# Optimization experiments

Hardware: AMD Instinct MI355X
Metric: run time of the kernel (lower is better)

Reference implementation:

```python
import jax, jax.numpy as jnp
import numpy as np

N = 100000      # nodes
E = 1600000     # edges (avg degree 16)
IN = 128
OUT = 256


def setup_inputs() -> dict:
    key = jax.random.key(0)
    ks = jax.random.split(key, 8)
    x = jax.random.normal(ks[0], (N, IN), dtype=jnp.float32)
    edge_index = jax.random.randint(ks[1], (2, E), 0, N, dtype=jnp.int64)
    # GCNConv weights (glorot-ish scale) and biases
    W1 = jax.random.normal(ks[2], (IN, OUT), dtype=jnp.float32) / np.float32(np.sqrt(IN))
    b1 = jnp.zeros((OUT,), jnp.float32)
    W2 = jax.random.normal(ks[3], (OUT, OUT), dtype=jnp.float32) / np.float32(np.sqrt(OUT))
    b2 = jnp.zeros((OUT,), jnp.float32)
    # projection Linear(IN, OUT)
    Wp = jax.random.normal(ks[4], (IN, OUT), dtype=jnp.float32) / np.float32(np.sqrt(IN))
    bp = jax.random.normal(ks[5], (OUT,), dtype=jnp.float32) * 0.01
    return {"x": x, "edge_index": edge_index, "W1": W1, "b1": b1,
            "W2": W2, "b2": b2, "Wp": Wp, "bp": bp}


def _gcn_conv(x, W, b, src, dst, n):
    """PyG GCNConv: D^{-1/2}(A+I)D^{-1/2} X W + b. src/dst already include self-loops."""
    xw = x @ W                                              # [n, out]
    ones = jnp.ones(src.shape[0], dtype=xw.dtype)
    deg = jax.ops.segment_sum(ones, dst, num_segments=n)    # in-degree incl. self-loop
    dinv = jnp.where(deg > 0, jax.lax.rsqrt(deg), 0.0)
    norm = dinv[src] * dinv[dst]                            # [e]
    msgs = xw[src] * norm[:, None]                          # gather + scale
    out = jax.ops.segment_sum(msgs, dst, num_segments=n)    # scatter-add
    return out + b


def reference(x, edge_index, W1, b1, W2, b2, Wp, bp):
    n = x.shape[0]
    loop = jnp.arange(n, dtype=edge_index.dtype)            # self-loops
    src = jnp.concatenate([edge_index[0], loop])
    dst = jnp.concatenate([edge_index[1], loop])
    out = jax.nn.relu(_gcn_conv(x, W1, b1, src, dst, n))
    out = _gcn_conv(out, W2, b2, src, dst, n)
    identity = x @ Wp + bp                                  # projection (IN != OUT)
    return jax.nn.relu(out + identity)
```

## Files before the change

kernel.cpp:

```cpp
#include <hip/hip_runtime.h>

#define NODES 100000
#define EDGES 1600000
#define FIN   128
#define FOUT  256
#define NBUCK 196
#define NBLKS 98

typedef __bf16 bf16;
typedef __bf16 bf16x8 __attribute__((ext_vector_type(8)));
typedef __bf16 bf16x4 __attribute__((ext_vector_type(4)));
typedef __bf16 bf16x2 __attribute__((ext_vector_type(2)));
typedef float  f32x4  __attribute__((ext_vector_type(4)));
typedef float  f32x2  __attribute__((ext_vector_type(2)));

__device__ __forceinline__ f32x2 bf2f(unsigned w) {
    f32x2 r;
    r[0] = __uint_as_float(w << 16);
    r[1] = __uint_as_float(w & 0xffff0000u);
    return r;
}

__device__ __forceinline__ void acc_u4(f32x2 a[4], uint4 w) {
    a[0] += bf2f(w.x); a[1] += bf2f(w.y);
    a[2] += bf2f(w.z); a[3] += bf2f(w.w);
}

__device__ __forceinline__ int edge_at(const int* __restrict__ ei, int which, int i,
                                       int is64) {
    if (is64) return ei[2 * (which * EDGES + i)];
    return ei[which * EDGES + i];
}

__global__ __launch_bounds__(256) void init_kernel(const void* __restrict__ x,
                                                   const int* __restrict__ ei,
                                                   int* __restrict__ zero0,
                                                   int* __restrict__ flags,
                                                   float* __restrict__ zpadA,
                                                   float* __restrict__ zpadB) {
    int b = blockIdx.x, t = threadIdx.x;
    if (b < 394) {
        int i = b * 256 + t;
        if (i < 100864) zero0[i] = 0;
        return;
    }
    zpadA[t] = 0.0f;
    zpadB[t] = 0.0f;
    __shared__ int s_f32_evidence;
    __shared__ int s_odd_nonzero;
    if (t == 0) { s_f32_evidence = 0; s_odd_nonzero = 0; }
    __syncthreads();
    const bf16* xb = (const bf16*)x;
    int local_f32 = 0;
    for (int i = t; i < 4096; i += 256) {
        float v = fabsf((float)xb[i]);
        if (!(v < 1e4f)) local_f32 = 1;
    }
    if (local_f32) atomicOr(&s_f32_evidence, 1);
    int local_odd = 0;
    for (int k = t; k < 1024; k += 256) {
        if (ei[2 * k + 1] != 0) local_odd = 1;
    }
    if (local_odd) atomicOr(&s_odd_nonzero, 1);
    __syncthreads();
    if (t == 0) {
        flags[0] = s_f32_evidence ? 0 : 1;
        flags[1] = s_odd_nonzero ? 0 : 1;
    }
}

__global__ __launch_bounds__(512) void degcnt_pack(const int* __restrict__ ei,
                                                   int* __restrict__ deg,
                                                   int* __restrict__ bhist,
                                                   const void* __restrict__ W1,
                                                   const void* __restrict__ W2,
                                                   const void* __restrict__ Wp,
                                                   const void* __restrict__ b1,
                                                   const void* __restrict__ b2,
                                                   const void* __restrict__ bp,
                                                   bf16* __restrict__ W1p, bf16* __restrict__ W2p,
                                                   bf16* __restrict__ Wpp, bf16* __restrict__ b1b,
                                                   bf16* __restrict__ b2b, bf16* __restrict__ bpb,
                                                   const int* __restrict__ flags) {
    if (blockIdx.x < 3125) {
        __shared__ int lh[256];
        int t = threadIdx.x;
        if (t < 256) lh[t] = 0;
        __syncthreads();
        int i = blockIdx.x * 512 + t;
        if (i < EDGES) {
            int is64 = flags[1];
            int s = edge_at(ei, 0, i, is64);
            int d = edge_at(ei, 1, i, is64);
            if (s >= 0 && s < NODES && d >= 0 && d < NODES) {
                atomicAdd(&deg[d], 1);
                atomicAdd(&lh[d >> 9], 1);
            }
        }
        __syncthreads();
        if (t < NBUCK && lh[t] > 0) atomicAdd(&bhist[t], lh[t]);
        return;
    }
    if (threadIdx.x >= 256) return;
    int fl = flags[0];
    int b = blockIdx.x - 3125;
    if (b < 512) {
        const void* W; bf16* Wo; int idx;
        if (b < 128)      { W = W1; Wo = W1p; idx = b * 256 + threadIdx.x; }
        else if (b < 384) { W = W2; Wo = W2p; idx = (b - 128) * 256 + threadIdx.x; }
        else              { W = Wp; Wo = Wpp; idx = (b - 384) * 256 + threadIdx.x; }
        int j    = idx & 7;
        int lane = (idx >> 3) & 63;
        int ct   = (idx >> 9) & 15;
        int kt   = idx >> 13;
        int k = kt * 32 + (lane >> 4) * 8 + j;
        int n = ct * 16 + (lane & 15);
        Wo[idx] = fl ? ((const bf16*)W)[k * 256 + n]
                     : (bf16)(((const float*)W)[k * 256 + n]);
    } else {
        const void* bb; bf16* bo;
        if (b == 512)      { bb = b1; bo = b1b; }
        else if (b == 513) { bb = b2; bo = b2b; }
        else               { bb = bp; bo = bpb; }
        int i = threadIdx.x;
        bo[i] = fl ? ((const bf16*)bb)[i] : (bf16)(((const float*)bb)[i]);
    }
}

__global__ __launch_bounds__(1024) void scan1(const int* __restrict__ deg,
                                              int* __restrict__ col_ptr,
                                              int* __restrict__ blksum, int n) {
    __shared__ int sm[1024];
    int t = threadIdx.x;
    int i = blockIdx.x * 1024 + t;
    int v = (i < n) ? deg[i] + 1 : 0;
    sm[t] = v;
    __syncthreads();
    for (int off = 1; off < 1024; off <<= 1) {
        int u = (t >= off) ? sm[t - off] : 0;
        __syncthreads();
        sm[t] += u;
        __syncthreads();
    }
    if (i <= n) col_ptr[i] = sm[t] - v;
    if (t == 1023) blksum[blockIdx.x] = sm[t];
}

#define EPB 4096
__global__ __launch_bounds__(256) void part_scan3(const int* __restrict__ ei,
                                                  const int* __restrict__ bhist,
                                                  int* __restrict__ bcur,
                                                  uint2* __restrict__ pairs,
                                                  const int* __restrict__ flags,
                                                  int* __restrict__ col_ptr,
                                                  const int* __restrict__ blk,
                                                  const int* __restrict__ deg,
                                                  float* __restrict__ dinv,
                                                  int* __restrict__ col_idx, int n) {
    if (blockIdx.x < 391) {
        __shared__ int lh[256], sc[256], lst[256], lcu[256], gb[256], bs[256];
        __shared__ uint2 stage[EPB];
        int t = threadIdx.x;
        int base = blockIdx.x * EPB;
        int is64 = flags[1];

        lh[t] = 0;
        __syncthreads();

        int es[16], ed[16];
#pragma unroll
        for (int j = 0; j < 16; ++j) {
            int i = base + j * 256 + t;
            int s = -1, d = -1;
            if (i < EDGES) {
                s = edge_at(ei, 0, i, is64);
                d = edge_at(ei, 1, i, is64);
                if (s < 0 || s >= NODES || d < 0 || d >= NODES) d = -1;
            }
            es[j] = s; ed[j] = d;
            if (d >= 0) atomicAdd(&lh[d >> 9], 1);
        }
        __syncthreads();
        sc[t] = lh[t];
        __syncthreads();
        for (int off = 1; off < 256; off <<= 1) {
            int u = (t >= off) ? sc[t - off] : 0;
            __syncthreads();
            sc[t] += u;
            __syncthreads();
        }
        int start = sc[t] - lh[t];
        lst[t] = start;
        lcu[t] = start;
        __syncthreads();
#pragma unroll
        for (int j = 0; j < 16; ++j) {
            if (ed[j] >= 0) {
                int p = atomicAdd(&lcu[ed[j] >> 9], 1);
                stage[p] = make_uint2((unsigned)es[j], (unsigned)ed[j]);
            }
        }
        __syncthreads();
        int v2 = (t < NBUCK) ? bhist[t] : 0;
        bs[t] = v2;
        __syncthreads();
        for (int off = 1; off < 256; off <<= 1) {
            int u = (t >= off) ? bs[t - off] : 0;
            __syncthreads();
            bs[t] += u;
            __syncthreads();
        }
        if (t < NBUCK && lh[t] > 0)
            gb[t] = (bs[t] - v2) + atomicAdd(&bcur[t], lh[t]);
        __syncthreads();
        int nval = sc[255];
        for (int slot = t; slot < nval; slot += 256) {
            uint2 e = stage[slot];
            int b = (int)(e.y >> 9);
            pairs[(size_t)gb[b] + (slot - lst[b])] = e;
        }
        return;
    }
    __shared__ int sb[128];
    int t = threadIdx.x;
    int sid = blockIdx.x - 391;
    int ov = 0;
    if (t < 128) { ov = (t < NBLKS) ? blk[t] : 0; sb[t] = ov; }
    __syncthreads();
    for (int off = 1; off < 128; off <<= 1) {
        int u = (t >= off && t < 128) ? sb[t - off] : 0;
        __syncthreads();
        if (t < 128) sb[t] += u;
        __syncthreads();
    }
    if (t < 128) sb[t] -= ov;
    __syncthreads();
    int i = sid * 256 + t;
    if (i <= n) {
        int v = col_ptr[i] + sb[i >> 10];
        col_ptr[i] = v;
        if (i < n) col_idx[v] = i;
    }
    if (i < n) dinv[i] = rsqrtf((float)deg[i] + 1.0f);
}

__global__ __launch_bounds__(256) void ff_proj(const uint2* __restrict__ pairs,
                                               const int* __restrict__ bhist,
                                               const int* __restrict__ col_ptr,
                                               int* __restrict__ col_idx,
                                               const void* __restrict__ Av,
                                               const bf16* __restrict__ Wpk,
                                               const float* __restrict__ dinv,
                                               const bf16* __restrict__ biasp,
                                               const bf16* __restrict__ bias2,
                                               void* __restrict__ outv,
                                               bf16* __restrict__ projb,
                                               int use_projb,
                                               bf16* __restrict__ Xs,
                                               const int* __restrict__ flags) {
    if (blockIdx.x < NBUCK) {
        __shared__ int lcur[512];
        __shared__ int bs2[256];
        int b = blockIdx.x;
        int t = threadIdx.x;
        int v2 = (t < NBUCK) ? bhist[t] : 0;
        bs2[t] = v2;
        __syncthreads();
        for (int off = 1; off < 256; off <<= 1) {
            int u = (t >= off) ? bs2[t - off] : 0;
            __syncthreads();
            bs2[t] += u;
            __syncthreads();
        }
        int be = bs2[b];
        int bb = be - bhist[b];
        int node = (b << 9) + t;
        lcur[t] = (node < NODES) ? col_ptr[node] + 1 : 0;
        int node2 = node + 256;
        lcur[t + 256] = (node2 < NODES) ? col_ptr[node2] + 1 : 0;
        __syncthreads();
        for (int i = bb + t; i < be; i += 256) {
            uint2 e = pairs[i];
            int pos = atomicAdd(&lcur[e.y & 511], 1);
            col_idx[pos] = (int)e.x;
        }
        return;
    }
    int a_f32 = (flags[0] == 0);
    int wave = threadIdx.x >> 6;
    int lane = threadIdx.x & 63;
    int row0 = (blockIdx.x - NBUCK) * 64;
    int lr = lane & 15;
    int lk = (lane >> 4) * 8;

    int arow[4];
    float di4[4];
#pragma unroll
    for (int rf = 0; rf < 4; ++rf) {
        int r = row0 + rf * 16 + lr;
        arow[rf] = r < NODES ? r : (NODES - 1);
        di4[rf] = dinv[arow[rf]];
    }

    f32x4 acc[4][4];
    f32x4 z = {0.f, 0.f, 0.f, 0.f};
#pragma unroll
    for (int i = 0; i < 4; ++i)
#pragma unroll
        for (int j = 0; j < 4; ++j) acc[i][j] = z;

    for (int kt = 0; kt < 4; ++kt) {
        bf16x8 af[4];
        if (!a_f32) {
            const bf16* Ab = (const bf16*)Av + kt * 32 + lk;
#pragma unroll
            for (int rf = 0; rf < 4; ++rf)
                af[rf] = *(const bf16x8*)(Ab + (size_t)arow[rf] * FIN);
        } else {
            const float* Af = (const float*)Av + kt * 32 + lk;
#pragma unroll
            for (int rf = 0; rf < 4; ++rf) {
                const float* p = Af + (size_t)arow[rf] * FIN;
                f32x4 lo = *(const f32x4*)p;
                f32x4 hi = *(const f32x4*)(p + 4);
                af[rf][0] = (bf16)lo[0]; af[rf][1] = (bf16)lo[1];
                af[rf][2] = (bf16)lo[2]; af[rf][3] = (bf16)lo[3];
                af[rf][4] = (bf16)hi[0]; af[rf][5] = (bf16)hi[1];
                af[rf][6] = (bf16)hi[2]; af[rf][7] = (bf16)hi[3];
            }
        }
#pragma unroll
        for (int rf = 0; rf < 4; ++rf) {
            bf16x8 xsv;
#pragma unroll
            for (int j = 0; j < 8; ++j) xsv[j] = (bf16)(di4[rf] * (float)af[rf][j]);
            *(bf16x8*)(Xs + (size_t)arow[rf] * FIN + kt * 32 + lk) = xsv;
        }
        const bf16* wb = Wpk + ((size_t)(kt * 16 + wave * 4) * 64 + lane) * 8;
        bf16x8 bfv[4];
#pragma unroll
        for (int cf = 0; cf < 4; ++cf)
            bfv[cf] = *(const bf16x8*)(wb + cf * 512);
#pragma unroll
        for (int rf = 0; rf < 4; ++rf)
#pragma unroll
            for (int cf = 0; cf < 4; ++cf)
                acc[rf][cf] = __builtin_amdgcn_mfma_f32_16x16x32_bf16(
                    af[rf], bfv[cf], acc[rf][cf], 0, 0, 0);
    }

    int rb = (lane >> 4) * 4;
#pragma unroll
    for (int rf = 0; rf < 4; ++rf) {
#pragma unroll
        for (int r = 0; r < 4; ++r) {
            int row = row0 + rf * 16 + rb + r;
            if (row >= NODES) continue;
#pragma unroll
            for (int cf = 0; cf < 4; ++cf) {
                int col = wave * 64 + cf * 16 + lr;
                float v = acc[rf][cf][r] + (float)biasp[col] + (float)bias2[col];
                size_t off = (size_t)row * 256 + col;
                if (a_f32) {
                    if (use_projb) projb[off] = (bf16)v;
                    else           ((float*)outv)[off] = v;
                } else {
                    ((bf16*)outv)[off] = (bf16)v;
                }
            }
        }
    }
}

__device__ __forceinline__ f32x2 sel_reduce4(f32x2 a[4], int rg) {
    f32x2 k0 = (rg & 2) ? a[2] : a[0];
    f32x2 k1 = (rg & 2) ? a[3] : a[1];
    f32x2 s0 = (rg & 2) ? a[0] : a[2];
    f32x2 s1 = (rg & 2) ? a[1] : a[3];
    f32x2 t;
    t[0] = __shfl_xor(s0[0], 32); t[1] = __shfl_xor(s0[1], 32); k0 += t;
    t[0] = __shfl_xor(s1[0], 32); t[1] = __shfl_xor(s1[1], 32); k1 += t;
    f32x2 c = (rg & 1) ? k1 : k0;
    f32x2 s = (rg & 1) ? k0 : k1;
    t[0] = __shfl_xor(s[0], 16); t[1] = __shfl_xor(s[1], 16); c += t;
    return c;
}

#define SMLD 264
__global__ __launch_bounds__(512) void g1conv(const int* __restrict__ col_ptr,
                                              const int* __restrict__ col_idx,
                                              const bf16* __restrict__ Xs,
                                              const float* __restrict__ dinv,
                                              const bf16* __restrict__ W1p,
                                              const bf16* __restrict__ W2p,
                                              const bf16* __restrict__ b1b,
                                              bf16* __restrict__ Y2) {
    __shared__ bf16 sm[64][SMLD];
    int wave = threadIdx.x >> 6;
    int lane = threadIdx.x & 63;
    int row0 = blockIdx.x * 64;
    int li = lane & 15;
    int rg = lane >> 4;

    const char* Xl = (const char*)Xs + li * 16;
    for (int k = 0; k < 8; ++k) {
        int node = row0 + wave * 8 + k;
        int nn = node < NODES ? node : (NODES - 1);
        int beg = col_ptr[nn], end = col_ptr[nn + 1];
        float di = dinv[nn];
        f32x2 a[4];
#pragma unroll
        for (int d = 0; d < 4; ++d) { a[d][0] = 0.f; a[d][1] = 0.f; }
        for (int chunk = beg; chunk < end; chunk += 64) {
            int gpos = chunk + lane;
            int idx = -2;
            if (gpos < end) idx = col_idx[gpos];
            int moff = idx << 8;
            int cnt = end - chunk; if (cnt > 64) cnt = 64;
            int j = 0;
            for (; j + 8 <= cnt; j += 8) {
                int so0 = __shfl(moff, j + rg);
                int so1 = __shfl(moff, j + 4 + rg);
                uint4 w0 = *(const uint4*)(Xl + so0);
                uint4 w1 = *(const uint4*)(Xl + so1);
                acc_u4(a, w0); acc_u4(a, w1);
            }
            for (; j < cnt; j += 4) {
                int so = __shfl(moff, j + rg);
                uint4 w = *(const uint4*)(Xl + so);
                acc_u4(a, w);
            }
        }
        f32x2 s = sel_reduce4(a, rg);
        bf16x2 o;
        o[0] = (bf16)(di * s[0]);
        o[1] = (bf16)(di * s[1]);
        *(bf16x2*)&sm[wave * 8 + k][li * 8 + rg * 2] = o;
    }
    __syncthreads();

    int wr = wave & 1;
    int wc = wave >> 1;
    int lr = li;
    int lk = rg * 8;
    f32x4 acc[2][4];
    f32x4 z = {0.f, 0.f, 0.f, 0.f};
#pragma unroll
    for (int i = 0; i < 2; ++i)
#pragma unroll
        for (int j = 0; j < 4; ++j) acc[i][j] = z;
    for (int kt = 0; kt < 4; ++kt) {
        bf16x8 af[2];
#pragma unroll
        for (int rf = 0; rf < 2; ++rf)
            af[rf] = *(const bf16x8*)&sm[wr * 32 + rf * 16 + lr][kt * 32 + lk];
        const bf16* wb = W1p + ((size_t)(kt * 16 + wc * 4) * 64 + lane) * 8;
        bf16x8 bfv[4];
#pragma unroll
        for (int cf = 0; cf < 4; ++cf)
            bfv[cf] = *(const bf16x8*)(wb + cf * 512);
#pragma unroll
        for (int rf = 0; rf < 2; ++rf)
#pragma unroll
            for (int cf = 0; cf < 4; ++cf)
                acc[rf][cf] = __builtin_amdgcn_mfma_f32_16x16x32_bf16(
                    af[rf], bfv[cf], acc[rf][cf], 0, 0, 0);
    }
    __syncthreads();

    int rb = rg * 4;
#pragma unroll
    for (int rf = 0; rf < 2; ++rf)
#pragma unroll
        for (int r = 0; r < 4; ++r) {
            int row = wr * 32 + rf * 16 + rb + r;
#pragma unroll
            for (int cf = 0; cf < 4; ++cf) {
                int col = wc * 64 + cf * 16 + lr;
                float v = acc[rf][cf][r] + (float)b1b[col];
                sm[row][col] = (bf16)fmaxf(v, 0.0f);
            }
        }
    __syncthreads();

#pragma unroll
    for (int i = 0; i < 2; ++i)
#pragma unroll
        for (int j = 0; j < 4; ++j) acc[i][j] = z;
    for (int kt = 0; kt < 8; ++kt) {
        bf16x8 af[2];
#pragma unroll
        for (int rf = 0; rf < 2; ++rf)
            af[rf] = *(const bf16x8*)&sm[wr * 32 + rf * 16 + lr][kt * 32 + lk];
        const bf16* wb = W2p + ((size_t)(kt * 16 + wc * 4) * 64 + lane) * 8;
        bf16x8 bfv[4];
#pragma unroll
        for (int cf = 0; cf < 4; ++cf)
            bfv[cf] = *(const bf16x8*)(wb + cf * 512);
#pragma unroll
        for (int rf = 0; rf < 2; ++rf)
#pragma unroll
            for (int cf = 0; cf < 4; ++cf)
                acc[rf][cf] = __builtin_amdgcn_mfma_f32_16x16x32_bf16(
                    af[rf], bfv[cf], acc[rf][cf], 0, 0, 0);
    }
#pragma unroll
    for (int rf = 0; rf < 2; ++rf)
#pragma unroll
        for (int r = 0; r < 4; ++r) {
            int row = row0 + wr * 32 + rf * 16 + rb + r;
            if (row >= NODES) continue;
            float di = dinv[row];
#pragma unroll
            for (int cf = 0; cf < 4; ++cf) {
                int col = wc * 64 + cf * 16 + lr;
                Y2[(size_t)row * 256 + col] = (bf16)(acc[rf][cf][r] * di);
            }
        }
}

__global__ __launch_bounds__(256) void gather2(const int* __restrict__ col_ptr,
                                               const int* __restrict__ col_idx,
                                               const bf16* __restrict__ Y2,
                                               const float* __restrict__ dinv,
                                               const bf16* __restrict__ projb,
                                               int use_projb,
                                               void* __restrict__ outv,
                                               const int* __restrict__ flags) {
    int io_f32 = (flags[0] == 0);
    int b = blockIdx.x;
    int slice = b & 1;
    int wave  = threadIdx.x >> 6;
    int wid   = (b >> 1) * 4 + wave;
    int lane  = threadIdx.x & 63;
    if (wid >= NODES) return;
    int beg = col_ptr[wid], end = col_ptr[wid + 1];
    int li = lane & 15;
    int rg = lane >> 4;
    int ch0 = slice * 128 + li * 8 + rg * 2;
    size_t obase = (size_t)wid * 256 + ch0;

    float di = dinv[wid];
    float pj0, pj1;
    if (io_f32) {
        if (use_projb) {
            bf16x2 p = *(const bf16x2*)(projb + obase);
            pj0 = (float)p[0]; pj1 = (float)p[1];
        } else {
            f32x2 p = *(const f32x2*)((const float*)outv + obase);
            pj0 = p[0]; pj1 = p[1];
        }
    } else {
        bf16x2 p = *(const bf16x2*)((const bf16*)outv + obase);
        pj0 = (float)p[0]; pj1 = (float)p[1];
    }

    const char* Yl = (const char*)Y2 + slice * 256 + li * 16;
    f32x2 acc2[4];
#pragma unroll
    for (int d = 0; d < 4; ++d) { acc2[d][0] = 0.f; acc2[d][1] = 0.f; }
    for (int chunk = beg; chunk < end; chunk += 64) {
        int gpos = chunk + lane;
        int idx = -2;
        if (gpos < end) idx = col_idx[gpos];
        int moff = idx << 9;
        int cnt = end - chunk; if (cnt > 64) cnt = 64;
        int j = 0;
        for (; j + 16 <= cnt; j += 16) {
            int so0 = __shfl(moff, j + rg);
            int so1 = __shfl(moff, j + 4 + rg);
            int so2 = __shfl(moff, j + 8 + rg);
            int so3 = __shfl(moff, j + 12 + rg);
            uint4 w0 = *(const uint4*)(Yl + so0);
            uint4 w1 = *(const uint4*)(Yl + so1);
            uint4 w2 = *(const uint4*)(Yl + so2);
            uint4 w3 = *(const uint4*)(Yl + so3);
            acc_u4(acc2, w0); acc_u4(acc2, w1);
            acc_u4(acc2, w2); acc_u4(acc2, w3);
        }
        for (; j < cnt; j += 4) {
            int so = __shfl(moff, j + rg);
            uint4 w = *(const uint4*)(Yl + so);
            acc_u4(acc2, w);
        }
    }
    f32x2 s = sel_reduce4(acc2, rg);
    float r0 = fmaxf(di * s[0] + pj0, 0.0f);
    float r1 = fmaxf(di * s[1] + pj1, 0.0f);

    if (io_f32) {
        f32x2 o; o[0] = r0; o[1] = r1;
        __builtin_nontemporal_store(o, (f32x2*)((float*)outv + obase));
    } else {
        bf16x2 o; o[0] = (bf16)r0; o[1] = (bf16)r1;
        __builtin_nontemporal_store(o, (bf16x2*)((bf16*)outv + obase));
    }
}

__global__ __launch_bounds__(256) void zero_out(bf16* out, int nelem) {
    int i = blockIdx.x * 256 + threadIdx.x;
    if (i < nelem) out[i] = (bf16)0.0f;
}

extern "C" void kernel_launch(void* const* d_in, const int* in_sizes, int n_in,
                              void* d_out, int out_size, void* d_ws, size_t ws_size,
                              hipStream_t stream) {
    const void* x   = d_in[0];
    const int*  ei  = (const int*)d_in[1];
    const void* W1  = d_in[2];
    const void* b1  = d_in[3];
    const void* W2  = d_in[4];
    const void* b2  = d_in[5];
    const void* Wp  = d_in[6];
    const void* bp  = d_in[7];

    const size_t CIDX_ALLOC = 6800384;
    const size_t NEEDED     = 85074432;
    const size_t NEEDED_BIG = NEEDED + 51200000;
    if (ws_size < NEEDED) {
        zero_out<<<(NODES * 256 + 255) / 256, 256, 0, stream>>>((bf16*)d_out, NODES * 256);
        return;
    }
    int use_projb = (ws_size >= NEEDED_BIG) ? 1 : 0;

    char* w = (char*)d_ws;
    int*   col_ptr = (int*)w;   w += 401408;
    int*   deg     = (int*)w;   w += 401408;
    int*   bhist   = (int*)w;   w += 1024;
    int*   bcur    = (int*)w;   w += 1024;
    float* dinv    = (float*)w; w += 401408;
    int*   blk     = (int*)w;   w += 1024;
    int*   flags   = (int*)w;   w += 1024;
    int*   col_idx = (int*)w;   w += CIDX_ALLOC;
    bf16*  W1p     = (bf16*)w;  w += 65536;
    bf16*  W2p     = (bf16*)w;  w += 131072;
    bf16*  Wpp     = (bf16*)w;  w += 65536;
    bf16*  b1b     = (bf16*)w;  w += 512;
    bf16*  b2b     = (bf16*)w;  w += 512;
    bf16*  bpb     = (bf16*)w;  w += 512;
    char*  zpadA   = w;         w += 1024;
    bf16*  Xs      = (bf16*)w;  w += 25600000;
    char*  zpadB   = w;         w += 1024;
    bf16*  Y2      = (bf16*)w;  w += 51200000;
    bf16*  projb   = (bf16*)w;
    uint2* pairs   = (uint2*)Y2;

    init_kernel<<<395, 256, 0, stream>>>(x, ei, deg, flags, (float*)zpadA, (float*)zpadB);

    degcnt_pack<<<3640, 512, 0, stream>>>(ei, deg, bhist, W1, W2, Wp, b1, b2, bp,
                                          W1p, W2p, Wpp, b1b, b2b, bpb, flags);

    scan1<<<NBLKS, 1024, 0, stream>>>(deg, col_ptr, blk, NODES);

    part_scan3<<<391 + 392, 256, 0, stream>>>(ei, bhist, bcur, pairs, flags,
                                              col_ptr, blk, deg, dinv, col_idx, NODES);

    ff_proj<<<NBUCK + (NODES + 63) / 64, 256, 0, stream>>>(
        pairs, bhist, col_ptr, col_idx,
        x, Wpp, dinv, bpb, b2b, d_out, projb, use_projb, Xs, flags);

    g1conv<<<(NODES + 63) / 64, 512, 0, stream>>>(col_ptr, col_idx, Xs, dinv,
                                                  W1p, W2p, b1b, Y2);

    gather2<<<((NODES + 3) / 4) * 2, 256, 0, stream>>>(col_ptr, col_idx, Y2, dinv,
                                                       projb, use_projb, d_out, flags);
}
```

Baseline: 574.9 us.

## Replace bucketed two-pass CSR build with direct atomic scatter into col_idx

```diff
diff --git a/kernel.cpp b/kernel.cpp
--- a/kernel.cpp
+++ b/kernel.cpp
@@ -4,7 +4,6 @@
 #define EDGES 1600000
 #define FIN   128
 #define FOUT  256
-#define NBUCK 196
 #define NBLKS 98
 
 typedef __bf16 bf16;
@@ -34,14 +33,13 @@
 
 __global__ __launch_bounds__(256) void init_kernel(const void* __restrict__ x,
                                                    const int* __restrict__ ei,
-                                                   int* __restrict__ zero0,
+                                                   int* __restrict__ deg,
                                                    int* __restrict__ flags,
                                                    float* __restrict__ zpadA,
                                                    float* __restrict__ zpadB) {
     int b = blockIdx.x, t = threadIdx.x;
-    if (b < 394) {
-        int i = b * 256 + t;
-        if (i < 100864) zero0[i] = 0;
+    if (b < 392) {
+        deg[b * 256 + t] = 0;
         return;
     }
     zpadA[t] = 0.0f;
@@ -71,7 +69,6 @@
 
 __global__ __launch_bounds__(512) void degcnt_pack(const int* __restrict__ ei,
                                                    int* __restrict__ deg,
-                                                   int* __restrict__ bhist,
                                                    const void* __restrict__ W1,
                                                    const void* __restrict__ W2,
                                                    const void* __restrict__ Wp,
@@ -83,22 +80,14 @@
                                                    bf16* __restrict__ b2b, bf16* __restrict__ bpb,
                                                    const int* __restrict__ flags) {
     if (blockIdx.x < 3125) {
-        __shared__ int lh[256];
-        int t = threadIdx.x;
-        if (t < 256) lh[t] = 0;
-        __syncthreads();
-        int i = blockIdx.x * 512 + t;
+        int i = blockIdx.x * 512 + threadIdx.x;
         if (i < EDGES) {
             int is64 = flags[1];
             int s = edge_at(ei, 0, i, is64);
             int d = edge_at(ei, 1, i, is64);
-            if (s >= 0 && s < NODES && d >= 0 && d < NODES) {
+            if (s >= 0 && s < NODES && d >= 0 && d < NODES)
                 atomicAdd(&deg[d], 1);
-                atomicAdd(&lh[d >> 9], 1);
-            }
-        }
-        __syncthreads();
-        if (t < NBUCK && lh[t] > 0) atomicAdd(&bhist[t], lh[t]);
+        }
         return;
     }
     if (threadIdx.x >= 256) return;
@@ -129,11 +118,13 @@
 
 __global__ __launch_bounds__(1024) void scan1(const int* __restrict__ deg,
                                               int* __restrict__ col_ptr,
-                                              int* __restrict__ blksum, int n) {
+                                              int* __restrict__ blksum,
+                                              float* __restrict__ dinv, int n) {
     __shared__ int sm[1024];
     int t = threadIdx.x;
     int i = blockIdx.x * 1024 + t;
     int v = (i < n) ? deg[i] + 1 : 0;
+    if (i < n) dinv[i] = rsqrtf((float)v);
     sm[t] = v;
     __syncthreads();
     for (int off = 1; off < 1024; off <<= 1) {
@@ -146,84 +137,12 @@
     if (t == 1023) blksum[blockIdx.x] = sm[t];
 }
 
-#define EPB 4096
-__global__ __launch_bounds__(256) void part_scan3(const int* __restrict__ ei,
-                                                  const int* __restrict__ bhist,
-                                                  int* __restrict__ bcur,
-                                                  uint2* __restrict__ pairs,
-                                                  const int* __restrict__ flags,
-                                                  int* __restrict__ col_ptr,
-                                                  const int* __restrict__ blk,
-                                                  const int* __restrict__ deg,
-                                                  float* __restrict__ dinv,
-                                                  int* __restrict__ col_idx, int n) {
-    if (blockIdx.x < 391) {
-        __shared__ int lh[256], sc[256], lst[256], lcu[256], gb[256], bs[256];
-        __shared__ uint2 stage[EPB];
-        int t = threadIdx.x;
-        int base = blockIdx.x * EPB;
-        int is64 = flags[1];
-
-        lh[t] = 0;
-        __syncthreads();
-
-        int es[16], ed[16];
-#pragma unroll
-        for (int j = 0; j < 16; ++j) {
-            int i = base + j * 256 + t;
-            int s = -1, d = -1;
-            if (i < EDGES) {
-                s = edge_at(ei, 0, i, is64);
-                d = edge_at(ei, 1, i, is64);
-                if (s < 0 || s >= NODES || d < 0 || d >= NODES) d = -1;
-            }
-            es[j] = s; ed[j] = d;
-            if (d >= 0) atomicAdd(&lh[d >> 9], 1);
-        }
-        __syncthreads();
-        sc[t] = lh[t];
-        __syncthreads();
-        for (int off = 1; off < 256; off <<= 1) {
-            int u = (t >= off) ? sc[t - off] : 0;
-            __syncthreads();
-            sc[t] += u;
-            __syncthreads();
-        }
-        int start = sc[t] - lh[t];
-        lst[t] = start;
-        lcu[t] = start;
-        __syncthreads();
-#pragma unroll
-        for (int j = 0; j < 16; ++j) {
-            if (ed[j] >= 0) {
-                int p = atomicAdd(&lcu[ed[j] >> 9], 1);
-                stage[p] = make_uint2((unsigned)es[j], (unsigned)ed[j]);
-            }
-        }
-        __syncthreads();
-        int v2 = (t < NBUCK) ? bhist[t] : 0;
-        bs[t] = v2;
-        __syncthreads();
-        for (int off = 1; off < 256; off <<= 1) {
-            int u = (t >= off) ? bs[t - off] : 0;
-            __syncthreads();
-            bs[t] += u;
-            __syncthreads();
-        }
-        if (t < NBUCK && lh[t] > 0)
-            gb[t] = (bs[t] - v2) + atomicAdd(&bcur[t], lh[t]);
-        __syncthreads();
-        int nval = sc[255];
-        for (int slot = t; slot < nval; slot += 256) {
-            uint2 e = stage[slot];
-            int b = (int)(e.y >> 9);
-            pairs[(size_t)gb[b] + (slot - lst[b])] = e;
-        }
-        return;
-    }
+__global__ __launch_bounds__(256) void scan3(int* __restrict__ col_ptr,
+                                             const int* __restrict__ blk,
+                                             int* __restrict__ col_idx,
+                                             int* __restrict__ cur, int n) {
     __shared__ int sb[128];
     int t = threadIdx.x;
-    int sid = blockIdx.x - 391;
     int ov = 0;
     if (t < 128) { ov = (t < NBLKS) ? blk[t] : 0; sb[t] = ov; }
     __syncthreads();
@@ -235,61 +154,51 @@
     }
     if (t < 128) sb[t] -= ov;
     __syncthreads();
-    int i = sid * 256 + t;
+    int i = blockIdx.x * 256 + t;
     if (i <= n) {
         int v = col_ptr[i] + sb[i >> 10];
         col_ptr[i] = v;
-        if (i < n) col_idx[v] = i;
-    }
-    if (i < n) dinv[i] = rsqrtf((float)deg[i] + 1.0f);
-}
-
-__global__ __launch_bounds__(256) void ff_proj(const uint2* __restrict__ pairs,
-                                               const int* __restrict__ bhist,
-                                               const int* __restrict__ col_ptr,
-                                               int* __restrict__ col_idx,
-                                               const void* __restrict__ Av,
-                                               const bf16* __restrict__ Wpk,
-                                               const float* __restrict__ dinv,
-                                               const bf16* __restrict__ biasp,
-                                               const bf16* __restrict__ bias2,
-                                               void* __restrict__ outv,
-                                               bf16* __restrict__ projb,
-                                               int use_projb,
-                                               bf16* __restrict__ Xs,
-                                               const int* __restrict__ flags) {
-    if (blockIdx.x < NBUCK) {
-        __shared__ int lcur[512];
-        __shared__ int bs2[256];
-        int b = blockIdx.x;
+        if (i < n) {
+            col_idx[v] = i;
+            cur[i] = v + 1;
+        }
+    }
+}
+
+__global__ __launch_bounds__(256) void scat_proj(const int* __restrict__ ei,
+                                                 int* __restrict__ cur,
+                                                 int* __restrict__ col_idx,
+                                                 const void* __restrict__ Av,
+                                                 const bf16* __restrict__ Wpk,
+                                                 const float* __restrict__ dinv,
+                                                 const bf16* __restrict__ biasp,
+                                                 const bf16* __restrict__ bias2,
+                                                 void* __restrict__ outv,
+                                                 bf16* __restrict__ projb,
+                                                 int use_projb,
+                                                 bf16* __restrict__ Xs,
+                                                 const int* __restrict__ flags) {
+    if (blockIdx.x < 3125) {
         int t = threadIdx.x;
-        int v2 = (t < NBUCK) ? bhist[t] : 0;
-        bs2[t] = v2;
-        __syncthreads();
-        for (int off = 1; off < 256; off <<= 1) {
-            int u = (t >= off) ? bs2[t - off] : 0;
-            __syncthreads();
-            bs2[t] += u;
-            __syncthreads();
-        }
-        int be = bs2[b];
-        int bb = be - bhist[b];
-        int node = (b << 9) + t;
-        lcur[t] = (node < NODES) ? col_ptr[node] + 1 : 0;
-        int node2 = node + 256;
-        lcur[t + 256] = (node2 < NODES) ? col_ptr[node2] + 1 : 0;
-        __syncthreads();
-        for (int i = bb + t; i < be; i += 256) {
-            uint2 e = pairs[i];
-            int pos = atomicAdd(&lcur[e.y & 511], 1);
-            col_idx[pos] = (int)e.x;
+        int is64 = flags[1];
+#pragma unroll
+        for (int u = 0; u < 2; ++u) {
+            int i = blockIdx.x * 512 + u * 256 + t;
+            if (i < EDGES) {
+                int s = edge_at(ei, 0, i, is64);
+                int d = edge_at(ei, 1, i, is64);
+                if (s >= 0 && s < NODES && d >= 0 && d < NODES) {
+                    int p = atomicAdd(&cur[d], 1);
+                    col_idx[p] = s;
+                }
+            }
         }
         return;
     }
     int a_f32 = (flags[0] == 0);
     int wave = threadIdx.x >> 6;
     int lane = threadIdx.x & 63;
-    int row0 = (blockIdx.x - NBUCK) * 64;
+    int row0 = (blockIdx.x - 3125) * 64;
     int lr = lane & 15;
     int lk = (lane >> 4) * 8;
 
@@ -418,12 +327,17 @@
             int moff = idx << 8;
             int cnt = end - chunk; if (cnt > 64) cnt = 64;
             int j = 0;
-            for (; j + 8 <= cnt; j += 8) {
+            for (; j + 16 <= cnt; j += 16) {
                 int so0 = __shfl(moff, j + rg);
                 int so1 = __shfl(moff, j + 4 + rg);
+                int so2 = __shfl(moff, j + 8 + rg);
+                int so3 = __shfl(moff, j + 12 + rg);
                 uint4 w0 = *(const uint4*)(Xl + so0);
                 uint4 w1 = *(const uint4*)(Xl + so1);
+                uint4 w2 = *(const uint4*)(Xl + so2);
+                uint4 w3 = *(const uint4*)(Xl + so3);
                 acc_u4(a, w0); acc_u4(a, w1);
+                acc_u4(a, w2); acc_u4(a, w3);
             }
             for (; j < cnt; j += 4) {
                 int so = __shfl(moff, j + rg);
@@ -626,8 +540,6 @@
     char* w = (char*)d_ws;
     int*   col_ptr = (int*)w;   w += 401408;
     int*   deg     = (int*)w;   w += 401408;
-    int*   bhist   = (int*)w;   w += 1024;
-    int*   bcur    = (int*)w;   w += 1024;
     float* dinv    = (float*)w; w += 401408;
     int*   blk     = (int*)w;   w += 1024;
     int*   flags   = (int*)w;   w += 1024;
@@ -643,21 +555,19 @@
     char*  zpadB   = w;         w += 1024;
     bf16*  Y2      = (bf16*)w;  w += 51200000;
     bf16*  projb   = (bf16*)w;
-    uint2* pairs   = (uint2*)Y2;
-
-    init_kernel<<<395, 256, 0, stream>>>(x, ei, deg, flags, (float*)zpadA, (float*)zpadB);
-
-    degcnt_pack<<<3640, 512, 0, stream>>>(ei, deg, bhist, W1, W2, Wp, b1, b2, bp,
+    int*   cur     = (int*)Y2;
+
+    init_kernel<<<393, 256, 0, stream>>>(x, ei, deg, flags, (float*)zpadA, (float*)zpadB);
+
+    degcnt_pack<<<3640, 512, 0, stream>>>(ei, deg, W1, W2, Wp, b1, b2, bp,
                                           W1p, W2p, Wpp, b1b, b2b, bpb, flags);
 
-    scan1<<<NBLKS, 1024, 0, stream>>>(deg, col_ptr, blk, NODES);
-
-    part_scan3<<<391 + 392, 256, 0, stream>>>(ei, bhist, bcur, pairs, flags,
-                                              col_ptr, blk, deg, dinv, col_idx, NODES);
-
-    ff_proj<<<NBUCK + (NODES + 63) / 64, 256, 0, stream>>>(
-        pairs, bhist, col_ptr, col_idx,
-        x, Wpp, dinv, bpb, b2b, d_out, projb, use_projb, Xs, flags);
+    scan1<<<NBLKS, 1024, 0, stream>>>(deg, col_ptr, blk, dinv, NODES);
+
+    scan3<<<392, 256, 0, stream>>>(col_ptr, blk, col_idx, cur, NODES);
+
+    scat_proj<<<3125 + (NODES + 63) / 64, 256, 0, stream>>>(
+        ei, cur, col_idx, x, Wpp, dinv, bpb, b2b, d_out, projb, use_projb, Xs, flags);
 
     g1conv<<<(NODES + 63) / 64, 512, 0, stream>>>(col_ptr, col_idx, Xs, dinv,
                                                   W1p, W2p, b1b, Y2);
```

Measured after the change: 652.0 us. 13.4% more time.
